# Optimization experiments

Measured on AMD Instinct MI355X. Metric: run time of the kernel, lower is better.

The kernel has to match this reference:

```python
import jax, jax.numpy as jnp
import numpy as np

B, S, H, L, NH, DH, V, FF, WD, W = 16, 512, 768, 12, 12, 64, 30522, 3072, 256, 255
T = S - 1


def layer_norm(x, s, b, eps=1e-12):
    m = jnp.mean(x, -1, keepdims=True)
    v = jnp.mean((x - m) ** 2, -1, keepdims=True)
    return (x - m) * jax.lax.rsqrt(v + eps) * s + b


def setup_inputs() -> dict:
    key = jax.random.key(0)
    ks = jax.random.split(key, 20)
    rng = np.random.RandomState(0)
    # ragged structure: words per sentence and wordpieces per word
    sent_lens = rng.randint(128, W + 1, size=B)
    token_lens = np.zeros((B, W), dtype=np.int32)
    for i in range(B):
        token_lens[i, : sent_lens[i]] = rng.randint(1, 3, size=sent_lens[i])
    bert_len = token_lens.sum(1)  # wordpieces per sentence (no CLS/SEP)
    attention_mask = (np.arange(S)[None, :] < (bert_len + 2)[:, None]).astype(np.int32)
    input_ids = rng.randint(0, V, size=(B, S)).astype(np.int32)
    sd = 0.02
    rn = lambda k, sh: jax.random.normal(k, sh, jnp.float32) * sd
    inp = {
        "input_ids": jnp.asarray(input_ids),
        "attention_mask": jnp.asarray(attention_mask),
        "token_lens": jnp.asarray(token_lens),
        "word_emb": rn(ks[0], (V, H)),
        "pos_emb": rn(ks[1], (S, H)),
        "type_emb": rn(ks[2], (2, H)),
        "emb_ln_s": jnp.ones((H,), jnp.float32),
        "emb_ln_b": jnp.zeros((H,), jnp.float32),
        "Wq": rn(ks[3], (L, H, H)), "bq": jnp.zeros((L, H), jnp.float32),
        "Wk": rn(ks[4], (L, H, H)), "bk": jnp.zeros((L, H), jnp.float32),
        "Wv": rn(ks[5], (L, H, H)), "bv": jnp.zeros((L, H), jnp.float32),
        "Wo": rn(ks[6], (L, H, H)), "bo": jnp.zeros((L, H), jnp.float32),
        "ln1_s": jnp.ones((L, H), jnp.float32), "ln1_b": jnp.zeros((L, H), jnp.float32),
        "W1": rn(ks[7], (L, H, FF)), "b1": jnp.zeros((L, FF), jnp.float32),
        "W2": rn(ks[8], (L, FF, H)), "b2": jnp.zeros((L, H), jnp.float32),
        "ln2_s": jnp.ones((L, H), jnp.float32), "ln2_b": jnp.zeros((L, H), jnp.float32),
        "proj_W": rn(ks[9], (H, WD)), "proj_b": jnp.zeros((WD,), jnp.float32),
    }
    return inp


def reference(input_ids, attention_mask, token_lens, word_emb, pos_emb, type_emb,
              emb_ln_s, emb_ln_b, Wq, bq, Wk, bk, Wv, bv, Wo, bo, ln1_s, ln1_b,
              W1, b1, W2, b2, ln2_s, ln2_b, proj_W, proj_b):
    # --- BERT embeddings ---
    h = word_emb[input_ids] + pos_emb[None, :, :] + type_emb[0][None, None, :]
    h = layer_norm(h, emb_ln_s, emb_ln_b)
    att_bias = (1.0 - attention_mask.astype(jnp.float32))[:, None, None, :] * -10000.0

    def block(h, p):
        wq, bq_, wk, bk_, wv, bv_, wo, bo_, l1s, l1b, w1, b1_, w2, b2_, l2s, l2b = p
        q = (h @ wq + bq_).reshape(B, S, NH, DH)
        k = (h @ wk + bk_).reshape(B, S, NH, DH)
        v = (h @ wv + bv_).reshape(B, S, NH, DH)
        scores = jnp.einsum('bqnd,bknd->bnqk', q, k) / np.float32(np.sqrt(DH)) + att_bias
        a = jax.nn.softmax(scores, axis=-1)
        ctx = jnp.einsum('bnqk,bknd->bqnd', a, v).reshape(B, S, H)
        h = layer_norm(h + ctx @ wo + bo_, l1s, l1b)
        f = jax.nn.gelu(h @ w1 + b1_, approximate=False) @ w2 + b2_
        h = layer_norm(h + f, l2s, l2b)
        return h, None

    h, _ = jax.lax.scan(block, h, (Wq, bq, Wk, bk, Wv, bv, Wo, bo, ln1_s, ln1_b,
                                   W1, b1, W2, b2, ln2_s, ln2_b))
    # drop [CLS], project to word_dims
    hid = h[:, 1:, :] @ proj_W + proj_b  # [B, T, WD]
    # --- ragged segment-mean merge (vectorized form of merge_embedding) ---
    cum = jnp.cumsum(token_lens, axis=1)  # [B, W]
    pos = jnp.arange(T)
    word_id = jnp.sum(pos[None, :, None] >= cum[:, None, :], axis=-1)  # token -> word
    valid = pos[None, :] < cum[:, -1][:, None]  # token within bert_len
    onehot = ((word_id[:, :, None] == jnp.arange(W)[None, None, :]) & valid[:, :, None]).astype(hid.dtype)
    sums = jnp.einsum('btw,btd->bwd', onehot, hid)  # [B, W, WD]
    means = sums / jnp.maximum(token_lens, 1)[:, :, None].astype(hid.dtype)
    word_masks = (token_lens > 0).astype(jnp.float32)  # [B, W]
    return means, word_masks
```

## Files before the change

### kernel.cpp

```cpp
#include <hip/hip_runtime.h>
#include <stdint.h>

#define B_ 16
#define S_ 512
#define H_ 768
#define L_ 12
#define NH_ 12
#define DH_ 64
#define FF_ 3072
#define WD_ 256
#define W_ 255
#define MTOK_ (B_*S_)
#define QKVN_ 2304
#define MPADR_ 128

typedef _Float16 f16;
typedef _Float16 f16x8 __attribute__((ext_vector_type(8)));
typedef _Float16 f16x4 __attribute__((ext_vector_type(4)));
typedef _Float16 f16x2 __attribute__((ext_vector_type(2)));
typedef float f32x4 __attribute__((ext_vector_type(4)));

#define SCHED_FENCE() __builtin_amdgcn_sched_barrier(0)

__device__ __forceinline__ float gelu_fast(float x) {
  float u = x * (1.0f + 0.044715f * x * x);
  float e = __expf(-1.5957691216f * u);
  return __fdividef(x, 1.0f + e);
}

__device__ __forceinline__ void gload16(const f16* g, f16* l) {
  __builtin_amdgcn_global_load_lds(
      (const __attribute__((address_space(1))) void*)g,
      (__attribute__((address_space(3))) void*)l, 16, 0, 0);
}

template<int BM, int BN, int ACT, int OUTF16, int BIAS, int QKVW, int SPLITK>
__global__ __launch_bounds__(256) void gemm2_k(
    const f16* __restrict__ A, const f16* __restrict__ Bm, void* __restrict__ Cv,
    const float* __restrict__ bias, f16* __restrict__ vTp,
    const int* __restrict__ rowmap, const int* __restrict__ meta,
    int lda, int ldb, int ldc, int K, float scale, long czoff)
{
  constexpr int MI = BM / 32;
  constexpr int NI = BN / 32;
  constexpr int LPW = BM / 32 + BN / 32;
  const int gx = gridDim.x;
  int flat = blockIdx.y * gx + blockIdx.x;
  const int nlive = (meta[1] / BM) * gx;
  if (flat >= nlive) return;
  {
    int q = nlive >> 3, r = nlive & 7;
    int xcd = flat & 7, idx = flat >> 3;
    flat = (xcd < r ? xcd * (q + 1) : r * (q + 1) + (xcd - r) * q) + idx;
  }
  const int row0 = (flat / gx) * BM;
  const int col0 = (flat % gx) * BN;
  const int z = (SPLITK > 1) ? blockIdx.z : 0;
  const int kc_len = K / SPLITK;
  A  += (size_t)z * kc_len;
  Bm += (size_t)z * kc_len;

  __shared__ __align__(16) f16 lA[2][BM * 64];
  __shared__ __align__(16) f16 lB[2][BN * 64];
  const int lane = threadIdx.x & 63;
  const int wave = threadIdx.x >> 6;
  const int wr = wave >> 1, wc = wave & 1;
  const int srow = lane >> 3;
  const int scol = lane & 7;
  const int cs = scol ^ srow;

  int arow[BM / 32];
#pragma unroll
  for (int i = 0; i < BM / 32; ++i)
    arow[i] = rowmap[row0 + (wave * (BM / 32) + i) * 8 + srow];

  auto stage = [&](int p, int k0) {
#pragma unroll
    for (int i = 0; i < BM / 32; ++i) {
      int seg = wave * (BM / 32) + i;
      gload16(&A[(size_t)arow[i] * lda + k0 + cs * 8], &lA[p][seg * 512]);
    }
#pragma unroll
    for (int i = 0; i < BN / 32; ++i) {
      int seg = wave * (BN / 32) + i;
      gload16(&Bm[(size_t)(col0 + seg * 8 + srow) * ldb + k0 + cs * 8], &lB[p][seg * 512]);
    }
  };

  f32x4 acc[MI][NI] = {};
  const int nt = kc_len >> 6;
  const int rl = lane & 15, g = lane >> 4;
  stage(0, 0);
  if (nt > 1) stage(1, 64);
  for (int t = 0; t < nt; ++t) {
    if (t < nt - 1) { asm volatile("s_waitcnt vmcnt(%0) lgkmcnt(0)" :: "i"(LPW) : "memory"); }
    else            { asm volatile("s_waitcnt vmcnt(0) lgkmcnt(0)" ::: "memory"); }
    SCHED_FENCE();
    __builtin_amdgcn_s_barrier();
    SCHED_FENCE();
    const int p = t & 1;
    __builtin_amdgcn_s_setprio(1);
#pragma unroll
    for (int c = 0; c < 2; ++c) {
      f16x8 af[MI], bf[NI];
#pragma unroll
      for (int mi = 0; mi < MI; ++mi) {
        int r = wr * (MI * 16) + mi * 16 + rl;
        int u = (c * 4 + g) ^ (r & 7);
        af[mi] = *(const f16x8*)&lA[p][r * 64 + u * 8];
      }
#pragma unroll
      for (int ni = 0; ni < NI; ++ni) {
        int r = wc * (NI * 16) + ni * 16 + rl;
        int u = (c * 4 + g) ^ (r & 7);
        bf[ni] = *(const f16x8*)&lB[p][r * 64 + u * 8];
      }
#pragma unroll
      for (int mi = 0; mi < MI; ++mi)
#pragma unroll
        for (int ni = 0; ni < NI; ++ni)
          acc[mi][ni] = __builtin_amdgcn_mfma_f32_16x16x32_f16(af[mi], bf[ni], acc[mi][ni], 0, 0, 0);
    }
    __builtin_amdgcn_s_setprio(0);
    SCHED_FENCE();
    asm volatile("s_waitcnt lgkmcnt(0)" ::: "memory");
    SCHED_FENCE();
    __builtin_amdgcn_s_barrier();
    SCHED_FENCE();
    if (t + 2 < nt) stage(p, (t + 2) * 64);
  }
  const int cl = lane & 15;
  const int rq = (lane >> 4) * 4;
#pragma unroll
  for (int mi = 0; mi < MI; ++mi) {
    const int4 rm4 = *(const int4*)&rowmap[row0 + wr * (MI * 16) + mi * 16 + rq];
    const int rows[4] = { rm4.x, rm4.y, rm4.z, rm4.w };
    const bool contig = (rm4.w == rm4.x + 3) && ((rm4.x & 3) == 0);
#pragma unroll
    for (int ni = 0; ni < NI; ++ni) {
      int col = col0 + wc * (NI * 16) + ni * 16 + cl;
      float bv = 0.f;
      if constexpr (BIAS) { if (SPLITK == 1 || z == 0) bv = bias[col]; }
      if constexpr (QKVW) {
        if (col >= 2 * H_) {
          int vc = col - 2 * H_;
          int h = vc >> 6, d = vc & 63;
          if (contig) {
            if (rm4.x < MTOK_) {
              int b = rm4.x >> 9, s = rm4.x & (S_ - 1);
              f16x4 o4;
#pragma unroll
              for (int r = 0; r < 4; ++r) o4[r] = (f16)(acc[mi][ni][r] * scale + bv);
              *(f16x4*)&vTp[(((size_t)(b * NH_ + h)) * DH_ + d) * S_ + s] = o4;
            }
          } else {
#pragma unroll
            for (int r = 0; r < 4; ++r) {
              int orow = rows[r];
              if (orow < MTOK_) {
                int b = orow >> 9, s = orow & (S_ - 1);
                vTp[(((size_t)(b * NH_ + h)) * DH_ + d) * S_ + s] = (f16)(acc[mi][ni][r] * scale + bv);
              }
            }
          }
          continue;
        }
      }
#pragma unroll
      for (int r = 0; r < 4; ++r) {
        float v = acc[mi][ni][r] * scale + bv;
        if constexpr (ACT == 1) v = gelu_fast(v);
        if constexpr (OUTF16) {
          ((f16*)Cv + (size_t)z * czoff)[(size_t)rows[r] * ldc + col] = (f16)v;
        } else {
          ((float*)Cv)[(size_t)rows[r] * ldc + col] = v;
        }
      }
    }
  }
}

__global__ __launch_bounds__(256) void fattn_k(
    const f16* __restrict__ qkv, const f16* __restrict__ vT,
    f16* __restrict__ ctx, const int* __restrict__ lenp)
{
  const int bh = blockIdx.x, qt = blockIdx.y;
  const int b = bh / NH_, h = bh - b * NH_;
  const int L = lenp[b];
  if ((qt << 7) >= L) return;
  const int nkt = (L + 63) >> 6;
  const int lane = threadIdx.x & 63, wave = threadIdx.x >> 6;
  const int rl = lane & 15, g = lane >> 4;
  const int srow = lane >> 3, scol = lane & 7;
  const int cs = scol ^ srow;

  __shared__ __align__(16) f16 lK[2][64 * 64];
  __shared__ __align__(16) f16 lV[2][64 * 64];
  __shared__ __align__(16) f16 lP[128 * 72];

  auto stage = [&](int p, int kt) {
#pragma unroll
    for (int i = 0; i < 2; ++i) {
      int seg = wave * 2 + i;
      int r = seg * 8 + srow;
      gload16(&qkv[((size_t)b * S_ + kt * 64 + r) * QKVN_ + H_ + h * DH_ + cs * 8], &lK[p][seg * 512]);
      gload16(&vT[((size_t)bh * DH_ + r) * S_ + kt * 64 + cs * 8], &lV[p][seg * 512]);
    }
  };

  const size_t qrow0 = (size_t)b * S_ + qt * 128 + wave * 32;
  f16x8 qf[2][2];
#pragma unroll
  for (int bq = 0; bq < 2; ++bq)
#pragma unroll
    for (int kc = 0; kc < 2; ++kc)
      qf[bq][kc] = *(const f16x8*)&qkv[(qrow0 + bq * 16 + rl) * QKVN_ + h * DH_ + kc * 32 + g * 8];

  float lsum[2] = {0.f, 0.f};
  f32x4 accO[2][4] = {};

  stage(0, 0);
  for (int kt = 0; kt < nkt; ++kt) {
    if (kt + 1 < nkt) {
      stage((kt + 1) & 1, kt + 1);
      asm volatile("s_waitcnt vmcnt(4) lgkmcnt(0)" ::: "memory");
    } else {
      asm volatile("s_waitcnt vmcnt(0) lgkmcnt(0)" ::: "memory");
    }
    SCHED_FENCE();
    __builtin_amdgcn_s_barrier();
    SCHED_FENCE();
    const int p = kt & 1;

    f32x4 accS[4][2] = {};
    __builtin_amdgcn_s_setprio(1);
#pragma unroll
    for (int kc = 0; kc < 2; ++kc) {
#pragma unroll
      for (int ak = 0; ak < 4; ++ak) {
        int row = ak * 16 + rl;
        int u = (kc * 4 + g) ^ (row & 7);
        f16x8 kf = *(const f16x8*)&lK[p][row * 64 + u * 8];
#pragma unroll
        for (int bq = 0; bq < 2; ++bq)
          accS[ak][bq] = __builtin_amdgcn_mfma_f32_16x16x32_f16(kf, qf[bq][kc], accS[ak][bq], 0, 0, 0);
      }
    }
    __builtin_amdgcn_s_setprio(0);

    const int kvb = kt * 64 + g * 4;
#pragma unroll
    for (int bq = 0; bq < 2; ++bq) {
      float pv[16];
      float ps = 0.f;
#pragma unroll
      for (int ak = 0; ak < 4; ++ak)
#pragma unroll
        for (int r = 0; r < 4; ++r) {
          float s = accS[ak][bq][r] * 0.125f;
          float pp = (kvb + ak * 16 + r < L) ? __expf(s) : 0.f;
          pv[ak * 4 + r] = pp;
          ps += pp;
        }
      ps += __shfl_xor(ps, 16);
      ps += __shfl_xor(ps, 32);
      lsum[bq] += ps;
      const int qrow = wave * 32 + bq * 16 + rl;
#pragma unroll
      for (int ak = 0; ak < 4; ++ak)
#pragma unroll
        for (int r2 = 0; r2 < 2; ++r2) {
          f16x2 pk = { (f16)pv[ak * 4 + r2 * 2], (f16)pv[ak * 4 + r2 * 2 + 1] };
          *(f16x2*)&lP[qrow * 72 + ak * 16 + g * 4 + r2 * 2] = pk;
        }
    }
    __builtin_amdgcn_s_setprio(1);
#pragma unroll
    for (int kc = 0; kc < 2; ++kc) {
      f16x8 pa[2], vf[4];
#pragma unroll
      for (int aq = 0; aq < 2; ++aq) {
        int prow = wave * 32 + aq * 16 + rl;
        pa[aq] = *(const f16x8*)&lP[prow * 72 + kc * 32 + g * 8];
      }
#pragma unroll
      for (int bd = 0; bd < 4; ++bd) {
        int vrow = bd * 16 + rl;
        int u = (kc * 4 + g) ^ (vrow & 7);
        vf[bd] = *(const f16x8*)&lV[p][vrow * 64 + u * 8];
      }
#pragma unroll
      for (int aq = 0; aq < 2; ++aq)
#pragma unroll
        for (int bd = 0; bd < 4; ++bd)
          accO[aq][bd] = __builtin_amdgcn_mfma_f32_16x16x32_f16(pa[aq], vf[bd], accO[aq][bd], 0, 0, 0);
    }
    __builtin_amdgcn_s_setprio(0);
    SCHED_FENCE();
    asm volatile("s_waitcnt lgkmcnt(0)" ::: "memory");
    SCHED_FENCE();
    __builtin_amdgcn_s_barrier();
    SCHED_FENCE();
  }

  float linv[2] = { 1.f / lsum[0], 1.f / lsum[1] };
  const size_t orow0 = (size_t)b * S_ + qt * 128 + wave * 32;
#pragma unroll
  for (int aq = 0; aq < 2; ++aq)
#pragma unroll
    for (int r = 0; r < 4; ++r) {
      float li = __shfl(linv[aq], (lane & 48) | (g * 4 + r));
      int q = aq * 16 + g * 4 + r;
#pragma unroll
      for (int bd = 0; bd < 4; ++bd)
        ctx[(orow0 + q) * H_ + h * DH_ + bd * 16 + rl] = (f16)(accO[aq][bd][r] * li);
    }
}

template<typename TI>
__global__ __launch_bounds__(256) void transpose_f16_k(
    const TI* __restrict__ in, f16* __restrict__ out,
    int ldin, int ldout, long i1, long o1)
{
  const int z = blockIdx.z;
  in  += (size_t)z * i1;
  out += (size_t)z * o1;
  __shared__ float t[32][33];
  const int kt = blockIdx.y * 32, nt = blockIdx.x * 32;
  const int tx = threadIdx.x & 31, tg = threadIdx.x >> 5;
#pragma unroll
  for (int i = 0; i < 4; ++i) {
    int k = tg * 4 + i;
    t[k][tx] = (float)in[(size_t)(kt + k) * ldin + nt + tx];
  }
  __syncthreads();
#pragma unroll
  for (int i = 0; i < 4; ++i) {
    int n = tg * 4 + i;
    out[(size_t)(nt + n) * ldout + kt + tx] = (f16)t[tx][n];
  }
}

__global__ void bias_cat_k(const float* __restrict__ bq, const float* __restrict__ bk,
                           const float* __restrict__ bv, float* __restrict__ out) {
  const int l = blockIdx.y;
  const int j = blockIdx.x * 256 + threadIdx.x;
  float v = (j < H_) ? bq[l * H_ + j] : (j < 2 * H_) ? bk[l * H_ + j - H_] : bv[l * H_ + j - 2 * H_];
  out[l * QKVN_ + j] = v;
}

__global__ __launch_bounds__(256) void embed_ln_k(
    const int* __restrict__ ids, const float* __restrict__ wemb,
    const float* __restrict__ pemb, const float* __restrict__ temb,
    const float* __restrict__ lns, const float* __restrict__ lnb,
    float* __restrict__ h32, f16* __restrict__ h16)
{
  const int row = blockIdx.x * 4 + (threadIdx.x >> 6);
  const int lane = threadIdx.x & 63;
  const int s = row & (S_ - 1);
  const float4* wp = (const float4*)(wemb + (size_t)ids[row] * H_);
  const float4* pp = (const float4*)(pemb + (size_t)s * H_);
  const float4* tp = (const float4*)temb;
  float4 x[3]; float sm = 0.f, sq = 0.f;
#pragma unroll
  for (int j = 0; j < 3; ++j) {
    int i4 = lane + 64 * j;
    float4 a = wp[i4], bb = pp[i4], c = tp[i4];
    float4 v; v.x = a.x + bb.x + c.x; v.y = a.y + bb.y + c.y;
    v.z = a.z + bb.z + c.z; v.w = a.w + bb.w + c.w;
    x[j] = v;
    sm += v.x + v.y + v.z + v.w;
    sq += v.x * v.x + v.y * v.y + v.z * v.z + v.w * v.w;
  }
#pragma unroll
  for (int o = 32; o > 0; o >>= 1) { sm += __shfl_xor(sm, o); sq += __shfl_xor(sq, o); }
  float mean = sm * (1.f / H_);
  float inv = rsqrtf(sq * (1.f / H_) - mean * mean + 1e-12f);
  float4* hw = (float4*)(h32 + (size_t)row * H_);
  f16* ho = h16 + (size_t)row * H_;
#pragma unroll
  for (int j = 0; j < 3; ++j) {
    int i4 = lane + 64 * j;
    float4 sc = ((const float4*)lns)[i4], bi = ((const float4*)lnb)[i4];
    float4 v = x[j], y;
    y.x = (v.x - mean) * inv * sc.x + bi.x;
    y.y = (v.y - mean) * inv * sc.y + bi.y;
    y.z = (v.z - mean) * inv * sc.z + bi.z;
    y.w = (v.w - mean) * inv * sc.w + bi.w;
    hw[i4] = y;
    f16x4 o4 = {(f16)y.x, (f16)y.y, (f16)y.z, (f16)y.w};
    *(f16x4*)&ho[i4 * 4] = o4;
  }
}

__global__ __launch_bounds__(256) void ln_res_k(
    float* __restrict__ h32, const f16* __restrict__ tmpA, const f16* __restrict__ tmpB,
    const float* __restrict__ lns, const float* __restrict__ lnb,
    f16* __restrict__ h16, const int* __restrict__ rowmap, const int* __restrict__ meta)
{
  const int crow = blockIdx.x * 4 + (threadIdx.x >> 6);
  if (crow >= meta[0]) return;
  const int row = rowmap[crow];
  const int lane = threadIdx.x & 63;
  const float4* hp = (const float4*)(h32 + (size_t)row * H_);
  const f16x4* ta = (const f16x4*)(tmpA + (size_t)row * H_);
  const f16x4* tb = (const f16x4*)(tmpB + (size_t)row * H_);
  float4 x[3]; float sm = 0.f, sq = 0.f;
#pragma unroll
  for (int j = 0; j < 3; ++j) {
    int i4 = lane + 64 * j;
    float4 a = hp[i4];
    f16x4 va = ta[i4], vb = tb[i4];
    float4 v;
    v.x = a.x + (float)va[0] + (float)vb[0];
    v.y = a.y + (float)va[1] + (float)vb[1];
    v.z = a.z + (float)va[2] + (float)vb[2];
    v.w = a.w + (float)va[3] + (float)vb[3];
    x[j] = v;
    sm += v.x + v.y + v.z + v.w;
    sq += v.x * v.x + v.y * v.y + v.z * v.z + v.w * v.w;
  }
#pragma unroll
  for (int o = 32; o > 0; o >>= 1) { sm += __shfl_xor(sm, o); sq += __shfl_xor(sq, o); }
  float mean = sm * (1.f / H_);
  float inv = rsqrtf(sq * (1.f / H_) - mean * mean + 1e-12f);
  float4* hw = (float4*)(h32 + (size_t)row * H_);
  f16* ho = h16 + (size_t)row * H_;
#pragma unroll
  for (int j = 0; j < 3; ++j) {
    int i4 = lane + 64 * j;
    float4 sc = ((const float4*)lns)[i4], bi = ((const float4*)lnb)[i4];
    float4 v = x[j], y;
    y.x = (v.x - mean) * inv * sc.x + bi.x;
    y.y = (v.y - mean) * inv * sc.y + bi.y;
    y.z = (v.z - mean) * inv * sc.z + bi.z;
    y.w = (v.w - mean) * inv * sc.w + bi.w;
    hw[i4] = y;
    f16x4 o4 = {(f16)y.x, (f16)y.y, (f16)y.z, (f16)y.w};
    *(f16x4*)&ho[i4 * 4] = o4;
  }
}

__global__ void len_k(const int* __restrict__ mask, int* __restrict__ len) {
  const int b = blockIdx.x;
  const int t = threadIdx.x;
  __shared__ int red[512];
  red[t] = mask[b * S_ + t]; __syncthreads();
  for (int o = 256; o > 0; o >>= 1) { if (t < o) red[t] += red[t + o]; __syncthreads(); }
  if (t == 0) len[b] = red[0];
}

__global__ void rowmap_k(const int* __restrict__ len, int* __restrict__ meta,
                         int* __restrict__ rowmap) {
  __shared__ int cum[17];
  if (threadIdx.x == 0) {
    int c = 0; cum[0] = 0;
    for (int b = 0; b < B_; ++b) { c += len[b]; cum[b + 1] = c; }
    meta[0] = c;
    meta[1] = (c + 127) & ~127;
  }
  __syncthreads();
  const int Mv = cum[16];
  for (int i = threadIdx.x; i < MTOK_ + MPADR_; i += 256) {
    int orig;
    if (i < Mv) {
      int b = 0;
#pragma unroll
      for (int t = 1; t <= 16; ++t) b += (i >= cum[t]) ? 1 : 0;
      orig = b * S_ + (i - cum[b]);
    } else {
      int d = i - Mv;
      orig = MTOK_ + (d < MPADR_ ? d : MPADR_ - 1);
    }
    rowmap[i] = orig;
  }
}

__global__ __launch_bounds__(256) void merge_k(
    const float* __restrict__ proj, const int* __restrict__ tl,
    float* __restrict__ means, float* __restrict__ masks)
{
  const int w = blockIdx.x, b = blockIdx.y;
  const int t = threadIdx.x;
  __shared__ int red[256];
  int part = 0;
  for (int j = t; j < w; j += 256) part += tl[b * W_ + j];
  red[t] = part; __syncthreads();
  for (int o = 128; o > 0; o >>= 1) { if (t < o) red[t] += red[t + o]; __syncthreads(); }
  const int start = red[0];
  const int len = tl[b * W_ + w];
  float s = 0.f;
  for (int l = 0; l < len; ++l)
    s += proj[((size_t)b * S_ + 1 + start + l) * WD_ + t];
  means[((size_t)b * W_ + w) * WD_ + t] = (len > 0) ? s / (float)len : 0.f;
  if (t == 0) masks[b * W_ + w] = (len > 0) ? 1.f : 0.f;
}

extern "C" void kernel_launch(void* const* d_in, const int* in_sizes, int n_in,
                              void* d_out, int out_size, void* d_ws, size_t ws_size,
                              hipStream_t stream)
{
  (void)in_sizes; (void)n_in; (void)out_size;
  const int*   ids   = (const int*)d_in[0];
  const int*   amask = (const int*)d_in[1];
  const int*   tlens = (const int*)d_in[2];
  const float* wemb  = (const float*)d_in[3];
  const float* pemb  = (const float*)d_in[4];
  const float* temb  = (const float*)d_in[5];
  const float* elns  = (const float*)d_in[6];
  const float* elnb  = (const float*)d_in[7];
  const float* Wq = (const float*)d_in[8];  const float* bq = (const float*)d_in[9];
  const float* Wk = (const float*)d_in[10]; const float* bk = (const float*)d_in[11];
  const float* Wv = (const float*)d_in[12]; const float* bv = (const float*)d_in[13];
  const float* Wo = (const float*)d_in[14]; const float* bo = (const float*)d_in[15];
  const float* l1s = (const float*)d_in[16]; const float* l1b = (const float*)d_in[17];
  const float* W1 = (const float*)d_in[18]; const float* b1 = (const float*)d_in[19];
  const float* W2 = (const float*)d_in[20]; const float* b2 = (const float*)d_in[21];
  const float* l2s = (const float*)d_in[22]; const float* l2b = (const float*)d_in[23];
  const float* pW = (const float*)d_in[24]; const float* pb = (const float*)d_in[25];

  const int MR = MTOK_ + MPADR_;
  char* ws = (char*)d_ws;
  size_t off = 0;
  auto alloc = [&](size_t n) { void* r = ws + off; off += (n + 255) & ~(size_t)255; return r; };
  float* h32   = (float*)alloc((size_t)MR * H_ * 4);
  f16*   h16   = (f16*)alloc((size_t)MR * H_ * 2);
  f16*   qkv   = (f16*)alloc((size_t)MR * QKVN_ * 2);
  f16*   ctx16 = (f16*)alloc((size_t)MR * H_ * 2);
  f16*   vT    = (f16*)alloc((size_t)B_ * NH_ * DH_ * S_ * 2);
  f16*   ff16  = (f16*)alloc((size_t)MR * FF_ * 2);
  f16*   tmp16 = (f16*)alloc((size_t)MR * H_ * 2 * 2);
  float* proj32 = (float*)alloc((size_t)MR * WD_ * 4);
  f16*   pwT   = (f16*)alloc((size_t)WD_ * H_ * 2);
  float* bqkv  = (float*)alloc((size_t)L_ * QKVN_ * 4);
  int*   lenb  = (int*)alloc(256);
  int*   meta  = (int*)alloc(256);
  int*   rowmap = (int*)alloc((size_t)MR * 4);
  f16*   tmp16b = tmp16 + (size_t)MR * H_;

  const size_t wqkv_sz = (size_t)QKVN_ * H_ * 2;
  const size_t wo_sz   = (size_t)H_ * H_ * 2;
  const size_t w1_sz   = (size_t)H_ * FF_ * 2;
  const size_t w2_sz   = (size_t)FF_ * H_ * 2;
  const size_t per_layer_w = wqkv_sz + wo_sz + w1_sz + w2_sz;
  const bool big = ws_size >= off + (size_t)L_ * per_layer_w + 8192;
  const int nz = big ? L_ : 1;
  f16* wqkv0 = (f16*)alloc((size_t)nz * wqkv_sz);
  f16* wo0   = (f16*)alloc((size_t)nz * wo_sz);
  f16* w10   = (f16*)alloc((size_t)nz * w1_sz);
  f16* w20   = (f16*)alloc((size_t)nz * w2_sz);

  len_k<<<B_, 512, 0, stream>>>(amask, lenb);
  rowmap_k<<<1, 256, 0, stream>>>(lenb, meta, rowmap);
  embed_ln_k<<<MTOK_ / 4, 256, 0, stream>>>(ids, wemb, pemb, temb, elns, elnb, h32, h16);
  transpose_f16_k<float><<<dim3(WD_/32, H_/32, 1), 256, 0, stream>>>(pW, pwT, WD_, H_, 0, 0);
  bias_cat_k<<<dim3(QKVN_/256, L_), 256, 0, stream>>>(bq, bk, bv, bqkv);

  if (big) {
    transpose_f16_k<float><<<dim3(H_/32, H_/32, L_), 256, 0, stream>>>(
        Wq, wqkv0,                   H_, H_, (long)H_*H_, (long)QKVN_*H_);
    transpose_f16_k<float><<<dim3(H_/32, H_/32, L_), 256, 0, stream>>>(
        Wk, wqkv0 + (size_t)H_*H_,   H_, H_, (long)H_*H_, (long)QKVN_*H_);
    transpose_f16_k<float><<<dim3(H_/32, H_/32, L_), 256, 0, stream>>>(
        Wv, wqkv0 + (size_t)2*H_*H_, H_, H_, (long)H_*H_, (long)QKVN_*H_);
    transpose_f16_k<float><<<dim3(H_/32, H_/32, L_), 256, 0, stream>>>(
        Wo, wo0, H_, H_, (long)H_*H_, (long)H_*H_);
    transpose_f16_k<float><<<dim3(FF_/32, H_/32, L_), 256, 0, stream>>>(
        W1, w10, FF_, H_, (long)H_*FF_, (long)H_*FF_);
    transpose_f16_k<float><<<dim3(H_/32, FF_/32, L_), 256, 0, stream>>>(
        W2, w20, H_, FF_, (long)FF_*H_, (long)FF_*H_);
  }

  for (int l = 0; l < L_; ++l) {
    f16* wqkv_l = wqkv0 + (size_t)(big ? l : 0) * QKVN_ * H_;
    f16* wo_l   = wo0   + (size_t)(big ? l : 0) * H_ * H_;
    f16* w1_l   = w10   + (size_t)(big ? l : 0) * H_ * FF_;
    f16* w2_l   = w20   + (size_t)(big ? l : 0) * FF_ * H_;
    if (!big) {
      transpose_f16_k<float><<<dim3(H_/32, H_/32, 1), 256, 0, stream>>>(
          Wq + (size_t)l*H_*H_, wqkv_l,                   H_, H_, 0, 0);
      transpose_f16_k<float><<<dim3(H_/32, H_/32, 1), 256, 0, stream>>>(
          Wk + (size_t)l*H_*H_, wqkv_l + (size_t)H_*H_,   H_, H_, 0, 0);
      transpose_f16_k<float><<<dim3(H_/32, H_/32, 1), 256, 0, stream>>>(
          Wv + (size_t)l*H_*H_, wqkv_l + (size_t)2*H_*H_, H_, H_, 0, 0);
      transpose_f16_k<float><<<dim3(H_/32, H_/32, 1), 256, 0, stream>>>(
          Wo + (size_t)l*H_*H_, wo_l, H_, H_, 0, 0);
      transpose_f16_k<float><<<dim3(FF_/32, H_/32, 1), 256, 0, stream>>>(
          W1 + (size_t)l*H_*FF_, w1_l, FF_, H_, 0, 0);
      transpose_f16_k<float><<<dim3(H_/32, FF_/32, 1), 256, 0, stream>>>(
          W2 + (size_t)l*FF_*H_, w2_l, H_, FF_, 0, 0);
    }
    gemm2_k<128,128,0,1,1,1,1><<<dim3(QKVN_/128, MTOK_/128, 1), 256, 0, stream>>>(
        h16, wqkv_l, qkv, bqkv + (size_t)l*QKVN_, vT, rowmap, meta, H_, H_, QKVN_, H_, 1.0f, 0);
    fattn_k<<<dim3(B_*NH_, S_/128), 256, 0, stream>>>(qkv, vT, ctx16, lenb);
    gemm2_k<64,128,0,1,1,0,2><<<dim3(H_/128, MTOK_/64, 2), 256, 0, stream>>>(
        ctx16, wo_l, tmp16, bo + (size_t)l*H_, nullptr, rowmap, meta, H_, H_, H_, H_, 1.0f, (long)MR * H_);
    ln_res_k<<<MTOK_/4, 256, 0, stream>>>(h32, tmp16, tmp16b, l1s + (size_t)l*H_, l1b + (size_t)l*H_, h16, rowmap, meta);
    gemm2_k<128,128,1,1,1,0,1><<<dim3(FF_/128, MTOK_/128, 1), 256, 0, stream>>>(
        h16, w1_l, ff16, b1 + (size_t)l*FF_, nullptr, rowmap, meta, H_, H_, FF_, H_, 1.0f, 0);
    gemm2_k<64,128,0,1,1,0,2><<<dim3(H_/128, MTOK_/64, 2), 256, 0, stream>>>(
        ff16, w2_l, tmp16, b2 + (size_t)l*H_, nullptr, rowmap, meta, FF_, FF_, H_, FF_, 1.0f, (long)MR * H_);
    ln_res_k<<<MTOK_/4, 256, 0, stream>>>(h32, tmp16, tmp16b, l2s + (size_t)l*H_, l2b + (size_t)l*H_, h16, rowmap, meta);
  }

  gemm2_k<64,64,0,0,1,0,1><<<dim3(WD_/64, MTOK_/64, 1), 256, 0, stream>>>(
      h16, pwT, proj32, pb, nullptr, rowmap, meta, H_, H_, WD_, H_, 1.0f, 0);
  merge_k<<<dim3(W_, B_), 256, 0, stream>>>(proj32, tlens,
      (float*)d_out, (float*)d_out + (size_t)B_ * W_ * WD_);
}
```

Before: 2.476 ms.

## Drop fp32 residual stream, single-buffer GEMM staging, fuse length/rowmap kernels

Several unrelated changes land together. The fp32 hidden-state copy is removed, so the residual stream lives only in fp16, which saves global traffic in the embedding and layernorm kernels but adds rounding error to the residual accumulation. The GEMM loses its double-buffered global-to-LDS prefetch and becomes a plain load/sync/compute loop, so load latency is no longer hidden. The len and rowmap kernels are merged into one launch, and the split-K output GEMMs move to 64x64 tiles.

```diff
diff --git a/kernel.cpp b/kernel.cpp
--- a/kernel.cpp
+++ b/kernel.cpp
@@ -43,7 +43,6 @@
 {
   constexpr int MI = BM / 32;
   constexpr int NI = BN / 32;
-  constexpr int LPW = BM / 32 + BN / 32;
   const int gx = gridDim.x;
   int flat = blockIdx.y * gx + blockIdx.x;
   const int nlive = (meta[1] / BM) * gx;
@@ -60,8 +59,8 @@
   A  += (size_t)z * kc_len;
   Bm += (size_t)z * kc_len;
 
-  __shared__ __align__(16) f16 lA[2][BM * 64];
-  __shared__ __align__(16) f16 lB[2][BN * 64];
+  __shared__ __align__(16) f16 lA[BM * 64];
+  __shared__ __align__(16) f16 lB[BN * 64];
   const int lane = threadIdx.x & 63;
   const int wave = threadIdx.x >> 6;
   const int wr = wave >> 1, wc = wave & 1;
@@ -74,32 +73,23 @@
   for (int i = 0; i < BM / 32; ++i)
     arow[i] = rowmap[row0 + (wave * (BM / 32) + i) * 8 + srow];
 
-  auto stage = [&](int p, int k0) {
-#pragma unroll
-    for (int i = 0; i < BM / 32; ++i) {
-      int seg = wave * (BM / 32) + i;
-      gload16(&A[(size_t)arow[i] * lda + k0 + cs * 8], &lA[p][seg * 512]);
-    }
-#pragma unroll
-    for (int i = 0; i < BN / 32; ++i) {
-      int seg = wave * (BN / 32) + i;
-      gload16(&Bm[(size_t)(col0 + seg * 8 + srow) * ldb + k0 + cs * 8], &lB[p][seg * 512]);
-    }
-  };
-
   f32x4 acc[MI][NI] = {};
   const int nt = kc_len >> 6;
   const int rl = lane & 15, g = lane >> 4;
-  stage(0, 0);
-  if (nt > 1) stage(1, 64);
   for (int t = 0; t < nt; ++t) {
-    if (t < nt - 1) { asm volatile("s_waitcnt vmcnt(%0) lgkmcnt(0)" :: "i"(LPW) : "memory"); }
-    else            { asm volatile("s_waitcnt vmcnt(0) lgkmcnt(0)" ::: "memory"); }
-    SCHED_FENCE();
-    __builtin_amdgcn_s_barrier();
-    SCHED_FENCE();
-    const int p = t & 1;
-    __builtin_amdgcn_s_setprio(1);
+    __syncthreads();
+    const int k0 = t * 64;
+#pragma unroll
+    for (int i = 0; i < BM / 32; ++i) {
+      int seg = wave * (BM / 32) + i;
+      gload16(&A[(size_t)arow[i] * lda + k0 + cs * 8], &lA[seg * 512]);
+    }
+#pragma unroll
+    for (int i = 0; i < BN / 32; ++i) {
+      int seg = wave * (BN / 32) + i;
+      gload16(&Bm[(size_t)(col0 + seg * 8 + srow) * ldb + k0 + cs * 8], &lB[seg * 512]);
+    }
+    __syncthreads();
 #pragma unroll
     for (int c = 0; c < 2; ++c) {
       f16x8 af[MI], bf[NI];
@@ -107,13 +97,13 @@
       for (int mi = 0; mi < MI; ++mi) {
         int r = wr * (MI * 16) + mi * 16 + rl;
         int u = (c * 4 + g) ^ (r & 7);
-        af[mi] = *(const f16x8*)&lA[p][r * 64 + u * 8];
+        af[mi] = *(const f16x8*)&lA[r * 64 + u * 8];
       }
 #pragma unroll
       for (int ni = 0; ni < NI; ++ni) {
         int r = wc * (NI * 16) + ni * 16 + rl;
         int u = (c * 4 + g) ^ (r & 7);
-        bf[ni] = *(const f16x8*)&lB[p][r * 64 + u * 8];
+        bf[ni] = *(const f16x8*)&lB[r * 64 + u * 8];
       }
 #pragma unroll
       for (int mi = 0; mi < MI; ++mi)
@@ -121,13 +111,6 @@
         for (int ni = 0; ni < NI; ++ni)
           acc[mi][ni] = __builtin_amdgcn_mfma_f32_16x16x32_f16(af[mi], bf[ni], acc[mi][ni], 0, 0, 0);
     }
-    __builtin_amdgcn_s_setprio(0);
-    SCHED_FENCE();
-    asm volatile("s_waitcnt lgkmcnt(0)" ::: "memory");
-    SCHED_FENCE();
-    __builtin_amdgcn_s_barrier();
-    SCHED_FENCE();
-    if (t + 2 < nt) stage(p, (t + 2) * 64);
   }
   const int cl = lane & 15;
   const int rq = (lane >> 4) * 4;
@@ -353,7 +336,7 @@
     const int* __restrict__ ids, const float* __restrict__ wemb,
     const float* __restrict__ pemb, const float* __restrict__ temb,
     const float* __restrict__ lns, const float* __restrict__ lnb,
-    float* __restrict__ h32, f16* __restrict__ h16)
+    f16* __restrict__ h16)
 {
   const int row = blockIdx.x * 4 + (threadIdx.x >> 6);
   const int lane = threadIdx.x & 63;
@@ -376,46 +359,42 @@
   for (int o = 32; o > 0; o >>= 1) { sm += __shfl_xor(sm, o); sq += __shfl_xor(sq, o); }
   float mean = sm * (1.f / H_);
   float inv = rsqrtf(sq * (1.f / H_) - mean * mean + 1e-12f);
-  float4* hw = (float4*)(h32 + (size_t)row * H_);
   f16* ho = h16 + (size_t)row * H_;
 #pragma unroll
   for (int j = 0; j < 3; ++j) {
     int i4 = lane + 64 * j;
     float4 sc = ((const float4*)lns)[i4], bi = ((const float4*)lnb)[i4];
-    float4 v = x[j], y;
-    y.x = (v.x - mean) * inv * sc.x + bi.x;
-    y.y = (v.y - mean) * inv * sc.y + bi.y;
-    y.z = (v.z - mean) * inv * sc.z + bi.z;
-    y.w = (v.w - mean) * inv * sc.w + bi.w;
-    hw[i4] = y;
-    f16x4 o4 = {(f16)y.x, (f16)y.y, (f16)y.z, (f16)y.w};
+    float4 v = x[j];
+    f16x4 o4 = {(f16)((v.x - mean) * inv * sc.x + bi.x),
+                (f16)((v.y - mean) * inv * sc.y + bi.y),
+                (f16)((v.z - mean) * inv * sc.z + bi.z),
+                (f16)((v.w - mean) * inv * sc.w + bi.w)};
     *(f16x4*)&ho[i4 * 4] = o4;
   }
 }
 
 __global__ __launch_bounds__(256) void ln_res_k(
-    float* __restrict__ h32, const f16* __restrict__ tmpA, const f16* __restrict__ tmpB,
+    f16* __restrict__ h16, const f16* __restrict__ tmpA, const f16* __restrict__ tmpB,
     const float* __restrict__ lns, const float* __restrict__ lnb,
-    f16* __restrict__ h16, const int* __restrict__ rowmap, const int* __restrict__ meta)
+    const int* __restrict__ rowmap, const int* __restrict__ meta)
 {
   const int crow = blockIdx.x * 4 + (threadIdx.x >> 6);
   if (crow >= meta[0]) return;
   const int row = rowmap[crow];
   const int lane = threadIdx.x & 63;
-  const float4* hp = (const float4*)(h32 + (size_t)row * H_);
+  const f16x4* hp = (const f16x4*)(h16 + (size_t)row * H_);
   const f16x4* ta = (const f16x4*)(tmpA + (size_t)row * H_);
   const f16x4* tb = (const f16x4*)(tmpB + (size_t)row * H_);
   float4 x[3]; float sm = 0.f, sq = 0.f;
 #pragma unroll
   for (int j = 0; j < 3; ++j) {
     int i4 = lane + 64 * j;
-    float4 a = hp[i4];
-    f16x4 va = ta[i4], vb = tb[i4];
+    f16x4 a = hp[i4], va = ta[i4], vb = tb[i4];
     float4 v;
-    v.x = a.x + (float)va[0] + (float)vb[0];
-    v.y = a.y + (float)va[1] + (float)vb[1];
-    v.z = a.z + (float)va[2] + (float)vb[2];
-    v.w = a.w + (float)va[3] + (float)vb[3];
+    v.x = (float)a[0] + (float)va[0] + (float)vb[0];
+    v.y = (float)a[1] + (float)va[1] + (float)vb[1];
+    v.z = (float)a[2] + (float)va[2] + (float)vb[2];
+    v.w = (float)a[3] + (float)va[3] + (float)vb[3];
     x[j] = v;
     sm += v.x + v.y + v.z + v.w;
     sq += v.x * v.x + v.y * v.y + v.z * v.z + v.w * v.w;
@@ -424,50 +403,49 @@
   for (int o = 32; o > 0; o >>= 1) { sm += __shfl_xor(sm, o); sq += __shfl_xor(sq, o); }
   float mean = sm * (1.f / H_);
   float inv = rsqrtf(sq * (1.f / H_) - mean * mean + 1e-12f);
-  float4* hw = (float4*)(h32 + (size_t)row * H_);
   f16* ho = h16 + (size_t)row * H_;
 #pragma unroll
   for (int j = 0; j < 3; ++j) {
     int i4 = lane + 64 * j;
     float4 sc = ((const float4*)lns)[i4], bi = ((const float4*)lnb)[i4];
-    float4 v = x[j], y;
-    y.x = (v.x - mean) * inv * sc.x + bi.x;
-    y.y = (v.y - mean) * inv * sc.y + bi.y;
-    y.z = (v.z - mean) * inv * sc.z + bi.z;
-    y.w = (v.w - mean) * inv * sc.w + bi.w;
-    hw[i4] = y;
-    f16x4 o4 = {(f16)y.x, (f16)y.y, (f16)y.z, (f16)y.w};
+    float4 v = x[j];
+    f16x4 o4 = {(f16)((v.x - mean) * inv * sc.x + bi.x),
+                (f16)((v.y - mean) * inv * sc.y + bi.y),
+                (f16)((v.z - mean) * inv * sc.z + bi.z),
+                (f16)((v.w - mean) * inv * sc.w + bi.w)};
     *(f16x4*)&ho[i4 * 4] = o4;
   }
 }
 
-__global__ void len_k(const int* __restrict__ mask, int* __restrict__ len) {
-  const int b = blockIdx.x;
+__global__ void lenmap_k(const int* __restrict__ mask, int* __restrict__ len,
+                         int* __restrict__ meta, int* __restrict__ rowmap) {
   const int t = threadIdx.x;
   __shared__ int red[512];
-  red[t] = mask[b * S_ + t]; __syncthreads();
-  for (int o = 256; o > 0; o >>= 1) { if (t < o) red[t] += red[t + o]; __syncthreads(); }
-  if (t == 0) len[b] = red[0];
-}
-
-__global__ void rowmap_k(const int* __restrict__ len, int* __restrict__ meta,
-                         int* __restrict__ rowmap) {
   __shared__ int cum[17];
-  if (threadIdx.x == 0) {
+  const int b = t >> 5, sl = t & 31;
+  int part = 0;
+#pragma unroll
+  for (int j = 0; j < 16; ++j) part += mask[b * S_ + sl + 32 * j];
+  red[t] = part; __syncthreads();
+  for (int o = 16; o > 0; o >>= 1) {
+    if (sl < o) red[t] += red[t + o];
+    __syncthreads();
+  }
+  if (t == 0) {
     int c = 0; cum[0] = 0;
-    for (int b = 0; b < B_; ++b) { c += len[b]; cum[b + 1] = c; }
+    for (int bb = 0; bb < B_; ++bb) { len[bb] = red[bb * 32]; c += red[bb * 32]; cum[bb + 1] = c; }
     meta[0] = c;
     meta[1] = (c + 127) & ~127;
   }
   __syncthreads();
   const int Mv = cum[16];
-  for (int i = threadIdx.x; i < MTOK_ + MPADR_; i += 256) {
+  for (int i = t; i < MTOK_ + MPADR_; i += 512) {
     int orig;
     if (i < Mv) {
-      int b = 0;
-#pragma unroll
-      for (int t = 1; t <= 16; ++t) b += (i >= cum[t]) ? 1 : 0;
-      orig = b * S_ + (i - cum[b]);
+      int bb = 0;
+#pragma unroll
+      for (int k = 1; k <= 16; ++k) bb += (i >= cum[k]) ? 1 : 0;
+      orig = bb * S_ + (i - cum[bb]);
     } else {
       int d = i - Mv;
       orig = MTOK_ + (d < MPADR_ ? d : MPADR_ - 1);
@@ -523,7 +501,6 @@
   char* ws = (char*)d_ws;
   size_t off = 0;
   auto alloc = [&](size_t n) { void* r = ws + off; off += (n + 255) & ~(size_t)255; return r; };
-  float* h32   = (float*)alloc((size_t)MR * H_ * 4);
   f16*   h16   = (f16*)alloc((size_t)MR * H_ * 2);
   f16*   qkv   = (f16*)alloc((size_t)MR * QKVN_ * 2);
   f16*   ctx16 = (f16*)alloc((size_t)MR * H_ * 2);
@@ -550,9 +527,8 @@
   f16* w10   = (f16*)alloc((size_t)nz * w1_sz);
   f16* w20   = (f16*)alloc((size_t)nz * w2_sz);
 
-  len_k<<<B_, 512, 0, stream>>>(amask, lenb);
-  rowmap_k<<<1, 256, 0, stream>>>(lenb, meta, rowmap);
-  embed_ln_k<<<MTOK_ / 4, 256, 0, stream>>>(ids, wemb, pemb, temb, elns, elnb, h32, h16);
+  lenmap_k<<<1, 512, 0, stream>>>(amask, lenb, meta, rowmap);
+  embed_ln_k<<<MTOK_ / 4, 256, 0, stream>>>(ids, wemb, pemb, temb, elns, elnb, h16);
   transpose_f16_k<float><<<dim3(WD_/32, H_/32, 1), 256, 0, stream>>>(pW, pwT, WD_, H_, 0, 0);
   bias_cat_k<<<dim3(QKVN_/256, L_), 256, 0, stream>>>(bq, bk, bv, bqkv);
 
@@ -593,14 +569,14 @@
     gemm2_k<128,128,0,1,1,1,1><<<dim3(QKVN_/128, MTOK_/128, 1), 256, 0, stream>>>(
         h16, wqkv_l, qkv, bqkv + (size_t)l*QKVN_, vT, rowmap, meta, H_, H_, QKVN_, H_, 1.0f, 0);
     fattn_k<<<dim3(B_*NH_, S_/128), 256, 0, stream>>>(qkv, vT, ctx16, lenb);
-    gemm2_k<64,128,0,1,1,0,2><<<dim3(H_/128, MTOK_/64, 2), 256, 0, stream>>>(
+    gemm2_k<64,64,0,1,1,0,2><<<dim3(H_/64, MTOK_/64, 2), 256, 0, stream>>>(
         ctx16, wo_l, tmp16, bo + (size_t)l*H_, nullptr, rowmap, meta, H_, H_, H_, H_, 1.0f, (long)MR * H_);
-    ln_res_k<<<MTOK_/4, 256, 0, stream>>>(h32, tmp16, tmp16b, l1s + (size_t)l*H_, l1b + (size_t)l*H_, h16, rowmap, meta);
+    ln_res_k<<<MTOK_/4, 256, 0, stream>>>(h16, tmp16, tmp16b, l1s + (size_t)l*H_, l1b + (size_t)l*H_, rowmap, meta);
     gemm2_k<128,128,1,1,1,0,1><<<dim3(FF_/128, MTOK_/128, 1), 256, 0, stream>>>(
         h16, w1_l, ff16, b1 + (size_t)l*FF_, nullptr, rowmap, meta, H_, H_, FF_, H_, 1.0f, 0);
-    gemm2_k<64,128,0,1,1,0,2><<<dim3(H_/128, MTOK_/64, 2), 256, 0, stream>>>(
+    gemm2_k<64,64,0,1,1,0,2><<<dim3(H_/64, MTOK_/64, 2), 256, 0, stream>>>(
         ff16, w2_l, tmp16, b2 + (size_t)l*H_, nullptr, rowmap, meta, FF_, FF_, H_, FF_, 1.0f, (long)MR * H_);
-    ln_res_k<<<MTOK_/4, 256, 0, stream>>>(h32, tmp16, tmp16b, l2s + (size_t)l*H_, l2b + (size_t)l*H_, h16, rowmap, meta);
+    ln_res_k<<<MTOK_/4, 256, 0, stream>>>(h16, tmp16, tmp16b, l2s + (size_t)l*H_, l2b + (size_t)l*H_, rowmap, meta);
   }
 
   gemm2_k<64,64,0,0,1,0,1><<<dim3(WD_/64, MTOK_/64, 1), 256, 0, stream>>>(
```

Result: faster. 2.284 ms (-7.8%).
